# Kernel optimization log

Measured on AMD Instinct MI355X. Metric: run time of the kernel, lower is better.

The kernel has to match this reference:

```python
import jax, jax.numpy as jnp
import numpy as np

TEMP = 0.05
EPS = 1e-8  # torch CosineSimilarity eps


def setup_inputs() -> dict:
    key = jax.random.key(0)
    k1, k2 = jax.random.split(key)
    feature1 = jax.random.normal(k1, (4096, 768), dtype=jnp.float32)
    feature2 = jax.random.normal(k2, (4096, 768), dtype=jnp.float32)
    return {"feature1": feature1, "feature2": feature2}


def reference(feature1, feature2):
    # cosine similarity via L2-normalize + GEMM (same math as broadcast cos_sim)
    n1 = feature1 / jnp.maximum(jnp.linalg.norm(feature1, axis=-1, keepdims=True), EPS)
    n2 = feature2 / jnp.maximum(jnp.linalg.norm(feature2, axis=-1, keepdims=True), EPS)
    logits = jnp.einsum("id,jd->ij", n1, n2) / TEMP  # [N, N]
    # cross-entropy with labels = arange(N) -> mean of -log_softmax diagonal
    logp = jax.nn.log_softmax(logits, axis=-1)
    loss = -jnp.mean(jnp.diagonal(logp))
    return loss
```

## Files before the change

### kernel.cpp

```cpp
#include <hip/hip_runtime.h>
#include <hip/hip_bf16.h>

#define NROWS 4096
#define DIM   768
#define NKT   6

typedef __attribute__((ext_vector_type(4))) float f32x4;

#define GAS(p) ((const __attribute__((address_space(1))) void*)(p))
#define SAS(p) ((__attribute__((address_space(3))) void*)(p))

__global__ __launch_bounds__(256) void k_norm(const float* __restrict__ f1,
                                              const float* __restrict__ f2,
                                              unsigned char* __restrict__ n1,
                                              unsigned char* __restrict__ n2,
                                              float* __restrict__ rowsum) {
    int b = blockIdx.x;
    int wid = threadIdx.x >> 6, lane = threadIdx.x & 63;
    int rowidx = b * 4 + wid;
    const float* src = (rowidx < NROWS) ? f1 : f2;
    unsigned char* dst = (rowidx < NROWS) ? n1 : n2;
    int row = rowidx & (NROWS - 1);
    const float4* srow = (const float4*)(src + (size_t)row * DIM);
    float4 v[3];
    float ss = 0.f;
#pragma unroll
    for (int r = 0; r < 3; ++r) {
        v[r] = srow[lane + 64 * r];
        ss += v[r].x * v[r].x + v[r].y * v[r].y + v[r].z * v[r].z + v[r].w * v[r].w;
    }
#pragma unroll
    for (int off = 32; off; off >>= 1) ss += __shfl_xor(ss, off);
    float inv8 = 8.0f / fmaxf(sqrtf(ss), 1e-8f);
    unsigned int* drow = (unsigned int*)(dst + (size_t)row * DIM);
#pragma unroll
    for (int r = 0; r < 3; ++r) {
        int w = __builtin_amdgcn_cvt_pk_fp8_f32(v[r].x * inv8, v[r].y * inv8, 0, false);
        w = __builtin_amdgcn_cvt_pk_fp8_f32(v[r].z * inv8, v[r].w * inv8, w, true);
        drow[lane + 64 * r] = (unsigned int)w;
    }
    if (b == 0) {
        float4 z = {0.f, 0.f, 0.f, 0.f};
#pragma unroll
        for (int i = 0; i < 4; ++i) ((float4*)rowsum)[threadIdx.x + 256 * i] = z;
    }
}


#define BARRIER __builtin_amdgcn_s_barrier()
#define WAIT_LGKM0 do { asm volatile("s_waitcnt lgkmcnt(0)" ::: "memory"); \
                        __builtin_amdgcn_sched_barrier(0); } while (0)
#define WAIT_VM8   do { asm volatile("s_waitcnt vmcnt(8)" ::: "memory"); \
                        __builtin_amdgcn_sched_barrier(0); } while (0)
#define PRIO1 __builtin_amdgcn_s_setprio(1)
#define PRIO0 __builtin_amdgcn_s_setprio(0)

__global__ __launch_bounds__(256, 2) void k_gemm_lse(const unsigned char* __restrict__ n1,
                                                     const unsigned char* __restrict__ n2,
                                                     float* __restrict__ rowsum,
                                                     float* __restrict__ diag) {
    __shared__ alignas(16) char ldsbuf[65536];
    char* ldsc = (char*)ldsbuf;

    int wg = blockIdx.x;
    int swz = (wg & 7) * 128 + (wg >> 3);
    int bi = swz >> 5;
    int bj = swz & 31;

    int tid = threadIdx.x;
    int wid = tid >> 6;
    int lane = tid & 63;
    int l15 = lane & 15, lk = lane >> 4;
    int wr = wid >> 1, wc = wid & 1;

    const unsigned char* abase = n1 + (size_t)bi * 128 * DIM;
    const unsigned char* bbase = n2 + (size_t)bj * 128 * DIM;

    const int stoff = (tid >> 3) * DIM + (((tid & 7) ^ ((tid >> 3) & 7)) * 16);

    const int h7 = l15 & 7;
    const int fbase = l15 * 128 + (lk & 1) * 8;
    int slotx[4];
#pragma unroll
    for (int j = 0; j < 4; ++j) slotx[j] = ((2 * j + (lk >> 1)) ^ h7) * 16;

    char* LAp[2] = { ldsc + wr * 8192,          ldsc + 32768 + wr * 8192 };
    char* LBp[2] = { ldsc + 16384 + wc * 8192,  ldsc + 32768 + 16384 + wc * 8192 };

#define STG1(b, isB, base, chunk, kt) do { \
    const unsigned char* _s = (base) + ((chunk) * 32) * DIM + (kt) * 128 + stoff; \
    char* _d = ldsc + (b) * 32768 + (isB) * 16384 + (chunk) * 4096 + tid * 16; \
    __builtin_amdgcn_global_load_lds(GAS(_s), SAS(_d), 16, 0, 0); \
} while (0)

#define STG8(b, kt) do { \
    STG1(b, 0, abase, 0, kt); STG1(b, 0, abase, 1, kt); \
    STG1(b, 0, abase, 2, kt); STG1(b, 0, abase, 3, kt); \
    STG1(b, 1, bbase, 0, kt); STG1(b, 1, bbase, 1, kt); \
    STG1(b, 1, bbase, 2, kt); STG1(b, 1, bbase, 3, kt); \
} while (0)

#define LDF(b, jp, Areg, Breg) do { \
    _Pragma("unroll") for (int m = 0; m < 4; ++m) \
    _Pragma("unroll") for (int jj = 0; jj < 2; ++jj) { \
        Areg[m][jj] = *(const long*)(LAp[b] + m * 2048 + fbase + slotx[(jp) * 2 + jj]); \
        Breg[m][jj] = *(const long*)(LBp[b] + m * 2048 + fbase + slotx[(jp) * 2 + jj]); \
    } } while (0)

#define MM32(Areg, Breg) do { _Pragma("unroll") for (int m = 0; m < 4; ++m) \
    _Pragma("unroll") for (int n = 0; n < 4; ++n) \
    _Pragma("unroll") for (int jj = 0; jj < 2; ++jj) { \
    f32x4* _c = &acc[m][n]; \
    *_c = __builtin_amdgcn_mfma_f32_16x16x32_fp8_fp8(Areg[m][jj], Breg[n][jj], *_c, 0, 0, 0); \
    } } while (0)

    long A0[4][2], B0[4][2], A1[4][2], B1[4][2];
    f32x4 acc[4][4] = {};

    STG8(0, 0);
    STG8(1, 1);
    WAIT_VM8;
    BARRIER;
    LDF(0, 0, A0, B0);

    for (int t = 0; t < NKT; t += 2) {
        int t2 = (t + 2 < NKT) ? t + 2 : t + 2 - NKT;
        int t3 = (t + 3 < NKT) ? t + 3 : t + 3 - NKT;
        WAIT_LGKM0;
        LDF(0, 1, A1, B1);
        PRIO1; MM32(A0, B0); PRIO0;
        WAIT_LGKM0;
        BARRIER;
        STG8(0, t2);
        PRIO1; MM32(A1, B1); PRIO0;
        WAIT_VM8;
        LDF(1, 0, A0, B0);
        BARRIER;
        WAIT_LGKM0;
        LDF(1, 1, A1, B1);
        PRIO1; MM32(A0, B0); PRIO0;
        WAIT_LGKM0;
        BARRIER;
        STG8(1, t3);
        PRIO1; MM32(A1, B1); PRIO0;
        WAIT_VM8;
        LDF(0, 0, A0, B0);
        BARRIER;
    }

    __syncthreads();

    const bool dblk = (bi == bj);
    const int rowb = bi * 128 + wr * 64;
    const int colb = bj * 128 + wc * 64;
#pragma unroll
    for (int mi = 0; mi < 4; ++mi) {
#pragma unroll
        for (int r = 0; r < 4; ++r) {
            float s = 0.f;
            int gi = rowb + mi * 16 + lk * 4 + r;
#pragma unroll
            for (int ni = 0; ni < 4; ++ni) {
                float v = acc[mi][ni][r] * (20.0f / 64.0f);
                s += __expf(v);
                if (dblk) {
                    int gj = colb + ni * 16 + l15;
                    if (gi == gj) diag[gi] = v;
                }
            }
#pragma unroll
            for (int off = 1; off < 16; off <<= 1) s += __shfl_xor(s, off);
            if (l15 == 0) atomicAdd(rowsum + gi, s);
        }
    }
}

__global__ __launch_bounds__(1024) void k_final(const float* __restrict__ rowsum,
                                                const float* __restrict__ diag,
                                                float* __restrict__ out) {
    int tid = threadIdx.x;
    float s = 0.f;
#pragma unroll
    for (int i = 0; i < 4; ++i) {
        int idx = tid + 1024 * i;
        s += logf(rowsum[idx]) - diag[idx];
    }
#pragma unroll
    for (int off = 32; off; off >>= 1) s += __shfl_xor(s, off);
    __shared__ float red[16];
    if ((tid & 63) == 0) red[tid >> 6] = s;
    __syncthreads();
    if (tid == 0) {
        float tot = 0.f;
#pragma unroll
        for (int i = 0; i < 16; ++i) tot += red[i];
        out[0] = tot * (1.0f / NROWS);
    }
}

extern "C" void kernel_launch(void* const* d_in, const int* in_sizes, int n_in,
                              void* d_out, int out_size, void* d_ws, size_t ws_size,
                              hipStream_t stream) {
    const float* f1 = (const float*)d_in[0];
    const float* f2 = (const float*)d_in[1];
    float* out = (float*)d_out;

    char* ws = (char*)d_ws;
    unsigned char* n1 = (unsigned char*)ws;
    unsigned char* n2 = n1 + (size_t)NROWS * DIM;
    float* rowsum = (float*)(ws + 2 * (size_t)NROWS * DIM);
    float* diag = rowsum + NROWS;

    k_norm<<<2048, 256, 0, stream>>>(f1, f2, n1, n2, rowsum);
    k_gemm_lse<<<1024, 256, 0, stream>>>(n1, n2, rowsum, diag);
    k_final<<<1, 1024, 0, stream>>>(rowsum, diag, out);
}
```

Baseline: 109.7 us.

## Replace hand-pipelined double-buffered GEMM loop with single-buffer loop at higher occupancy

The explicit double-buffered LDS pipeline in the fp8 GEMM is removed. It relied on manual vmcnt/lgkmcnt waits, barriers and s_setprio. In its place is a simple per-k-tile loop that stages one 32KB tile, synchronizes, runs the MFMAs and synchronizes again. Halving LDS and raising launch bounds to 4 workgroups per CU is meant to hide load latency through occupancy rather than intra-wave prefetch. The risk is that each workgroup now stalls on every tile load, and the extra barriers may outweigh the gain from more resident workgroups.

```diff
diff --git a/kernel.cpp b/kernel.cpp
--- a/kernel.cpp
+++ b/kernel.cpp
@@ -46,20 +46,11 @@
     }
 }
 
-
-#define BARRIER __builtin_amdgcn_s_barrier()
-#define WAIT_LGKM0 do { asm volatile("s_waitcnt lgkmcnt(0)" ::: "memory"); \
-                        __builtin_amdgcn_sched_barrier(0); } while (0)
-#define WAIT_VM8   do { asm volatile("s_waitcnt vmcnt(8)" ::: "memory"); \
-                        __builtin_amdgcn_sched_barrier(0); } while (0)
-#define PRIO1 __builtin_amdgcn_s_setprio(1)
-#define PRIO0 __builtin_amdgcn_s_setprio(0)
-
-__global__ __launch_bounds__(256, 2) void k_gemm_lse(const unsigned char* __restrict__ n1,
+__global__ __launch_bounds__(256, 4) void k_gemm_lse(const unsigned char* __restrict__ n1,
                                                      const unsigned char* __restrict__ n2,
                                                      float* __restrict__ rowsum,
                                                      float* __restrict__ diag) {
-    __shared__ alignas(16) char ldsbuf[65536];
+    __shared__ alignas(16) char ldsbuf[32768];
     char* ldsc = (char*)ldsbuf;
 
     int wg = blockIdx.x;
@@ -84,71 +75,41 @@
 #pragma unroll
     for (int j = 0; j < 4; ++j) slotx[j] = ((2 * j + (lk >> 1)) ^ h7) * 16;
 
-    char* LAp[2] = { ldsc + wr * 8192,          ldsc + 32768 + wr * 8192 };
-    char* LBp[2] = { ldsc + 16384 + wc * 8192,  ldsc + 32768 + 16384 + wc * 8192 };
+    const char* LAp = ldsc + wr * 8192;
+    const char* LBp = ldsc + 16384 + wc * 8192;
 
-#define STG1(b, isB, base, chunk, kt) do { \
+#define STG1(isB, base, chunk, kt) do { \
     const unsigned char* _s = (base) + ((chunk) * 32) * DIM + (kt) * 128 + stoff; \
-    char* _d = ldsc + (b) * 32768 + (isB) * 16384 + (chunk) * 4096 + tid * 16; \
+    char* _d = ldsc + (isB) * 16384 + (chunk) * 4096 + tid * 16; \
     __builtin_amdgcn_global_load_lds(GAS(_s), SAS(_d), 16, 0, 0); \
 } while (0)
 
-#define STG8(b, kt) do { \
-    STG1(b, 0, abase, 0, kt); STG1(b, 0, abase, 1, kt); \
-    STG1(b, 0, abase, 2, kt); STG1(b, 0, abase, 3, kt); \
-    STG1(b, 1, bbase, 0, kt); STG1(b, 1, bbase, 1, kt); \
-    STG1(b, 1, bbase, 2, kt); STG1(b, 1, bbase, 3, kt); \
-} while (0)
-
-#define LDF(b, jp, Areg, Breg) do { \
-    _Pragma("unroll") for (int m = 0; m < 4; ++m) \
-    _Pragma("unroll") for (int jj = 0; jj < 2; ++jj) { \
-        Areg[m][jj] = *(const long*)(LAp[b] + m * 2048 + fbase + slotx[(jp) * 2 + jj]); \
-        Breg[m][jj] = *(const long*)(LBp[b] + m * 2048 + fbase + slotx[(jp) * 2 + jj]); \
-    } } while (0)
-
-#define MM32(Areg, Breg) do { _Pragma("unroll") for (int m = 0; m < 4; ++m) \
-    _Pragma("unroll") for (int n = 0; n < 4; ++n) \
-    _Pragma("unroll") for (int jj = 0; jj < 2; ++jj) { \
-    f32x4* _c = &acc[m][n]; \
-    *_c = __builtin_amdgcn_mfma_f32_16x16x32_fp8_fp8(Areg[m][jj], Breg[n][jj], *_c, 0, 0, 0); \
-    } } while (0)
-
-    long A0[4][2], B0[4][2], A1[4][2], B1[4][2];
     f32x4 acc[4][4] = {};
 
-    STG8(0, 0);
-    STG8(1, 1);
-    WAIT_VM8;
-    BARRIER;
-    LDF(0, 0, A0, B0);
-
-    for (int t = 0; t < NKT; t += 2) {
-        int t2 = (t + 2 < NKT) ? t + 2 : t + 2 - NKT;
-        int t3 = (t + 3 < NKT) ? t + 3 : t + 3 - NKT;
-        WAIT_LGKM0;
-        LDF(0, 1, A1, B1);
-        PRIO1; MM32(A0, B0); PRIO0;
-        WAIT_LGKM0;
-        BARRIER;
-        STG8(0, t2);
-        PRIO1; MM32(A1, B1); PRIO0;
-        WAIT_VM8;
-        LDF(1, 0, A0, B0);
-        BARRIER;
-        WAIT_LGKM0;
-        LDF(1, 1, A1, B1);
-        PRIO1; MM32(A0, B0); PRIO0;
-        WAIT_LGKM0;
-        BARRIER;
-        STG8(1, t3);
-        PRIO1; MM32(A1, B1); PRIO0;
-        WAIT_VM8;
-        LDF(0, 0, A0, B0);
-        BARRIER;
+    for (int t = 0; t < NKT; ++t) {
+        STG1(0, abase, 0, t); STG1(0, abase, 1, t);
+        STG1(0, abase, 2, t); STG1(0, abase, 3, t);
+        STG1(1, bbase, 0, t); STG1(1, bbase, 1, t);
+        STG1(1, bbase, 2, t); STG1(1, bbase, 3, t);
+        __syncthreads();
+#pragma unroll
+        for (int j = 0; j < 4; ++j) {
+            long Af[4], Bf[4];
+#pragma unroll
+            for (int m = 0; m < 4; ++m)
+                Af[m] = *(const long*)(LAp + m * 2048 + fbase + slotx[j]);
+#pragma unroll
+            for (int n = 0; n < 4; ++n)
+                Bf[n] = *(const long*)(LBp + n * 2048 + fbase + slotx[j]);
+#pragma unroll
+            for (int m = 0; m < 4; ++m)
+#pragma unroll
+                for (int n = 0; n < 4; ++n)
+                    acc[m][n] = __builtin_amdgcn_mfma_f32_16x16x32_fp8_fp8(
+                                    Af[m], Bf[n], acc[m][n], 0, 0, 0);
+        }
+        __syncthreads();
     }
-
-    __syncthreads();
 
     const bool dblk = (bi == bj);
     const int rowb = bi * 128 + wr * 64;
```

After: 100.8 us. -8.1%, faster.
